# Kernel tuning notes

Measured on AMD Instinct MI355X. Metric: run time of the kernel, lower is better.

Reference implementation:

```python
import jax, jax.numpy as jnp
import numpy as np

D, N, L = 1024, 128, 128
B, S = 4, 4096

def setup_inputs() -> dict:
    key = jax.random.key(0)
    kx, kq, kk, kv = jax.random.split(key, 4)
    x = jax.random.normal(kx, (B, S, D), dtype=jnp.float32)
    # nn.Linear(d, n, bias=False) weight has shape [n, d]; y = x @ W.T
    Wq = jax.random.normal(kq, (N, D), dtype=jnp.float32) * (1.0 / np.sqrt(D))
    Wk = jax.random.normal(kk, (N, D), dtype=jnp.float32) * (1.0 / np.sqrt(D))
    Wv = jax.random.normal(kv, (L, D), dtype=jnp.float32) * (1.0 / np.sqrt(D))
    return {"x": x, "Wq": Wq, "Wk": Wk, "Wv": Wv}

def reference(x, Wq, Wk, Wv):
    scale = jnp.sqrt(jnp.asarray(D, dtype=x.dtype))  # self.d = sqrt(d) in source
    q = jnp.einsum('bsd,nd->bsn', x, Wq)  # [B,S,N]
    k = jnp.einsum('bsd,nd->bsn', x, Wk)  # [B,S,N]
    v = jnp.einsum('bsd,ld->bsl', x, Wv)  # [B,S,L]
    scores = jnp.einsum('bqn,bkn->bqk', q, k) / scale  # [B,S,S]
    a = jax.nn.softmax(scores, axis=-1)
    return jnp.einsum('bqk,bkl->bql', a, v)  # [B,S,L]
```

## Files before the change

### kernel.cpp

```cpp
#include <hip/hip_runtime.h>
#include <stdint.h>

typedef __attribute__((ext_vector_type(8))) _Float16 f16x8;
typedef __attribute__((ext_vector_type(4))) float f32x4;
typedef __attribute__((ext_vector_type(2))) float f32x2;

#define S_ 4096
#define D_ 1024
#define NROWS 16384
#define QSCALE 0.045084220f
#define EXP2(x) __builtin_amdgcn_exp2f(x)

__global__ __launch_bounds__(256) void cvtw(
    const float* __restrict__ Wq, const float* __restrict__ Wk,
    const float* __restrict__ Wv, _Float16* __restrict__ Wh)
{
  int i = (blockIdx.x * 256 + threadIdx.x) * 8;
  const float* src = (i < 131072) ? Wq : ((i < 262144) ? Wk : Wv);
  int off = i & 131071;
  f32x4 a = *(const f32x4*)(src + off);
  f32x4 b = *(const f32x4*)(src + off + 4);
  f16x8 h;
  #pragma unroll
  for (int j = 0; j < 4; ++j) { h[j] = (_Float16)a[j]; h[j + 4] = (_Float16)b[j]; }
  *(f16x8*)(Wh + i) = h;
}

__global__ __launch_bounds__(256) void gemm_qkv(
    const float* __restrict__ x, const _Float16* __restrict__ Wh,
    _Float16* __restrict__ qk, _Float16* __restrict__ vt)
{
  __shared__ char smem[32768];
  char* Ab[2] = { smem,        smem + 16384 };
  char* Bb[2] = { smem + 8192, smem + 24576 };
  const int tid  = threadIdx.x;
  const int lane = tid & 63, wid = tid >> 6;
  const int g = lane >> 4, l15 = lane & 15;
  const int m0 = blockIdx.x * 64;
  const int by = blockIdx.y;

  const char* pA[2];
  #pragma unroll
  for (int it = 0; it < 2; ++it) {
    int G = it * 256 + tid, row = G >> 3, gg = (G & 7) ^ (row & 7);
    pA[it] = (const char*)x + (size_t)(m0 + row) * 4096 + gg * 16;
  }
  const char* pB[2];
  #pragma unroll
  for (int it = 0; it < 2; ++it) {
    int d = it * 256 + tid;
    int rowhi = d >> 4, tt = (d & 15) ^ (rowhi & 15);
    int row = rowhi * 4 + (tt >> 2), gg = tt & 3;
    pB[it] = (const char*)(Wh + (size_t)by * 131072 + (size_t)row * 1024) + gg * 16;
  }

#define GSTAGE(bi) do {                                                        \
    _Pragma("unroll")                                                          \
    for (int it_ = 0; it_ < 2; ++it_) {                                        \
      __builtin_amdgcn_global_load_lds(pA[it_],                                \
          Ab[bi] + it_ * 4096 + wid * 1024, 16, 0, 0);                         \
      pA[it_] += 128;                                                          \
      __builtin_amdgcn_global_load_lds(pB[it_],                                \
          Bb[bi] + it_ * 4096 + wid * 1024, 16, 0, 0);                         \
      pB[it_] += 64;                                                           \
    }                                                                          \
  } while (0)

  f32x4 acc[4][2] = {};

#define GCOMPUTE(bi) do {                                                      \
    f16x8 af[4], bg[2];                                                        \
    _Pragma("unroll")                                                          \
    for (int mt = 0; mt < 4; ++mt) {                                           \
      int row = mt * 16 + l15;                                                 \
      const char* base = Ab[bi] + row * 128;                                   \
      f32x4 a0 = *(const f32x4*)(base + (((2 * g    ) ^ (row & 7)) << 4));     \
      f32x4 a1 = *(const f32x4*)(base + (((2 * g + 1) ^ (row & 7)) << 4));     \
      _Pragma("unroll")                                                        \
      for (int i = 0; i < 4; ++i) {                                            \
        af[mt][i] = (_Float16)a0[i]; af[mt][i + 4] = (_Float16)a1[i];          \
      }                                                                        \
    }                                                                          \
    _Pragma("unroll")                                                          \
    for (int nt = 0; nt < 2; ++nt) {                                           \
      int row = wid * 32 + nt * 16 + l15;                                      \
      int byte = ((row >> 2) * 256) +                                          \
                 (((((row & 3) << 2) | g) ^ ((row >> 2) & 15)) << 4);          \
      bg[nt] = *(const f16x8*)(Bb[bi] + byte);                                 \
    }                                                                          \
    __builtin_amdgcn_s_setprio(1);                                             \
    _Pragma("unroll")                                                          \
    for (int mt = 0; mt < 4; ++mt)                                             \
      _Pragma("unroll")                                                        \
      for (int nt = 0; nt < 2; ++nt)                                           \
        acc[mt][nt] = __builtin_amdgcn_mfma_f32_16x16x32_f16(af[mt], bg[nt],   \
                                                             acc[mt][nt], 0, 0, 0); \
    __builtin_amdgcn_s_setprio(0);                                             \
  } while (0)

  GSTAGE(0);
  __syncthreads();
  for (int t = 0; t < 32; t += 2) {
    GSTAGE(1);
    GCOMPUTE(0);
    __syncthreads();
    if (t + 2 < 32) GSTAGE(0);
    GCOMPUTE(1);
    __syncthreads();
  }

  if (by < 2) {
    const float sc = (by == 0) ? QSCALE : 1.0f;
    #pragma unroll
    for (int mt = 0; mt < 4; ++mt)
      #pragma unroll
      for (int nt = 0; nt < 2; ++nt)
        #pragma unroll
        for (int r = 0; r < 4; ++r) {
          int row = m0 + mt * 16 + (g << 2) + r;
          int col = by * 128 + wid * 32 + nt * 16 + l15;
          qk[(size_t)row * 256 + col] = (_Float16)(acc[mt][nt][r] * sc);
        }
  } else {
    _Float16* T = (_Float16*)smem;
    #pragma unroll
    for (int mt = 0; mt < 4; ++mt)
      #pragma unroll
      for (int nt = 0; nt < 2; ++nt)
        #pragma unroll
        for (int r = 0; r < 4; ++r)
          T[(mt * 16 + (g << 2) + r) * 128 + wid * 32 + nt * 16 + l15] =
              (_Float16)acc[mt][nt][r];
    __syncthreads();
    const int b = m0 >> 12, s_base = m0 & 4095;
    #pragma unroll
    for (int it = 0; it < 4; ++it) {
      int Wn = it * 256 + tid;
      int f = Wn >> 3, gran = Wn & 7;
      int kk = gran >> 2, q = gran & 3;
      f16x8 v;
      #pragma unroll
      for (int i = 0; i < 8; ++i) {
        int h = i >> 2, j = i & 3;
        v[i] = T[(kk * 32 + h * 16 + q * 4 + j) * 128 + f];
      }
      *(f16x8*)((char*)vt + (size_t)(b * 128 + f) * 8192 + s_base * 2 + gran * 16) = v;
    }
  }
#undef GSTAGE
#undef GCOMPUTE
}

__global__ __launch_bounds__(256, 2) void attn(const _Float16* __restrict__ qk,
                                               const _Float16* __restrict__ vt,
                                               _Float16* __restrict__ pO,
                                               float* __restrict__ pml,
                                               int ntiles)
{
  __shared__ _Float16 K0l[64 * 128], K1l[64 * 128];
  __shared__ _Float16 V0l[64 * 128], V1l[64 * 128];
  const int tid  = threadIdx.x;
  const int lane = tid & 63, wid = tid >> 6;
  const int g = lane >> 4, l15 = lane & 15;
  const int b  = blockIdx.y;
  const int q0 = blockIdx.x * 128;
  const int split = blockIdx.z;
  const int kv_begin = split * (ntiles * 64);

  f16x8 qf0[4], qf1[4];
  {
    const size_t qr0 = (size_t)(b * S_ + q0 + wid * 32 + l15) * 256;
    #pragma unroll
    for (int kk = 0; kk < 4; ++kk) {
      qf0[kk] = *(const f16x8*)(qk + qr0 + kk * 32 + g * 8);
      qf1[kk] = *(const f16x8*)(qk + qr0 + 16 * 256 + kk * 32 + g * 8);
    }
  }

  const char* gK[4]; const char* gV[4];
  #pragma unroll
  for (int it = 0; it < 4; ++it) {
    int G = it * 256 + tid;
    int row = G >> 4, ch = G & 15;
    gK[it] = (const char*)qk + (size_t)(b * S_ + kv_begin + row) * 512 + 256 +
             (((ch << 4)) ^ ((row & 15) << 4));
    int f = G >> 3, c = G & 7;
    gV[it] = (const char*)vt + (size_t)(b * 128 + f) * 8192 + (kv_begin >> 6) * 128 +
             ((c ^ (f & 7)) << 4);
  }

#define STAGE(Kb, Vb) do {                                                          \
    _Pragma("unroll")                                                               \
    for (int it_ = 0; it_ < 4; ++it_) {                                             \
      __builtin_amdgcn_global_load_lds(gK[it_],                                     \
          (char*)(Kb) + (it_ * 256 + wid * 64) * 16, 16, 0, 0);                     \
      __builtin_amdgcn_global_load_lds(gV[it_],                                     \
          (char*)(Vb) + (it_ * 256 + wid * 64) * 16, 16, 0, 0);                     \
      gK[it_] += 32768; gV[it_] += 128;                                             \
    }                                                                               \
  } while (0)

  f32x4 oa0[8] = {}, oa1[8] = {};
  float m0r = -1e30f, l0r = 0.f, m1r = -1e30f, l1r = 0.f;

#define COMPUTE(Kb, Vb) do {                                                        \
    f32x4 s0[4] = {}, s1[4] = {};                                                   \
    __builtin_amdgcn_s_setprio(1);                                                  \
    _Pragma("unroll")                                                               \
    for (int kk = 0; kk < 4; ++kk) {                                                \
      const char* kb = (const char*)(Kb) + l15 * 256 +                              \
                       (((kk << 6) | (g << 4)) ^ (l15 << 4));                       \
      _Pragma("unroll")                                                             \
      for (int kvt = 0; kvt < 4; ++kvt) {                                           \
        f16x8 kf = *(const f16x8*)(kb + kvt * 4096);                                \
        s0[kvt] = __builtin_amdgcn_mfma_f32_16x16x32_f16(kf, qf0[kk], s0[kvt],      \
                                                         0, 0, 0);                  \
        s1[kvt] = __builtin_amdgcn_mfma_f32_16x16x32_f16(kf, qf1[kk], s1[kvt],      \
                                                         0, 0, 0);                  \
      }                                                                             \
    }                                                                               \
    __builtin_amdgcn_s_setprio(0);                                                  \
    float p0 = fmaxf(                                                               \
        fmaxf(fmaxf(fmaxf(s0[0][0], s0[0][1]), fmaxf(s0[0][2], s0[0][3])),          \
              fmaxf(fmaxf(s0[1][0], s0[1][1]), fmaxf(s0[1][2], s0[1][3]))),         \
        fmaxf(fmaxf(fmaxf(s0[2][0], s0[2][1]), fmaxf(s0[2][2], s0[2][3])),          \
              fmaxf(fmaxf(s0[3][0], s0[3][1]), fmaxf(s0[3][2], s0[3][3]))));        \
    float p1 = fmaxf(                                                               \
        fmaxf(fmaxf(fmaxf(s1[0][0], s1[0][1]), fmaxf(s1[0][2], s1[0][3])),          \
              fmaxf(fmaxf(s1[1][0], s1[1][1]), fmaxf(s1[1][2], s1[1][3]))),         \
        fmaxf(fmaxf(fmaxf(s1[2][0], s1[2][1]), fmaxf(s1[2][2], s1[2][3])),          \
              fmaxf(fmaxf(s1[3][0], s1[3][1]), fmaxf(s1[3][2], s1[3][3]))));        \
    p0 = fmaxf(p0, __shfl_xor(p0, 16)); p0 = fmaxf(p0, __shfl_xor(p0, 32));         \
    p1 = fmaxf(p1, __shfl_xor(p1, 16)); p1 = fmaxf(p1, __shfl_xor(p1, 32));         \
    if (!__all((p0 - m0r <= 8.0f) && (p1 - m1r <= 8.0f))) {                         \
      float mn0 = fmaxf(m0r, p0), mn1 = fmaxf(m1r, p1);                             \
      float c0 = EXP2(m0r - mn0), c1 = EXP2(m1r - mn1);                             \
      l0r *= c0; m0r = mn0; l1r *= c1; m1r = mn1;                                   \
      _Pragma("unroll")                                                             \
      for (int r = 0; r < 4; ++r) {                                                 \
        int ad = ((g << 2) + r) << 2;                                               \
        float cr0 = __builtin_bit_cast(float,                                       \
            __builtin_amdgcn_ds_bpermute(ad, __builtin_bit_cast(int, c0)));         \
        float cr1 = __builtin_bit_cast(float,                                       \
            __builtin_amdgcn_ds_bpermute(ad, __builtin_bit_cast(int, c1)));         \
        _Pragma("unroll")                                                           \
        for (int ft = 0; ft < 8; ++ft) {                                            \
          oa0[ft][r] *= cr0; oa1[ft][r] *= cr1;                                     \
        }                                                                           \
      }                                                                             \
    }                                                                               \
    float ps0 = 0.f, ps1 = 0.f;                                                     \
    f16x8 pa0[2], pa1[2];                                                           \
    _Pragma("unroll")                                                               \
    for (int k2 = 0; k2 < 2; ++k2)                                                  \
      _Pragma("unroll")                                                             \
      for (int i = 0; i < 8; ++i) {                                                 \
        float e0 = EXP2(s0[2 * k2 + (i >> 2)][i & 3] - m0r);                        \
        float e1 = EXP2(s1[2 * k2 + (i >> 2)][i & 3] - m1r);                        \
        ps0 += e0; ps1 += e1;                                                       \
        pa0[k2][i] = (_Float16)e0; pa1[k2][i] = (_Float16)e1;                       \
      }                                                                             \
    ps0 += __shfl_xor(ps0, 16); ps0 += __shfl_xor(ps0, 32);                         \
    ps1 += __shfl_xor(ps1, 16); ps1 += __shfl_xor(ps1, 32);                         \
    l0r += ps0; l1r += ps1;                                                         \
    __builtin_amdgcn_s_setprio(1);                                                  \
    _Pragma("unroll")                                                               \
    for (int k2 = 0; k2 < 2; ++k2) {                                                \
      const char* vb = (const char*)(Vb) + l15 * 128 +                              \
                       (((k2 << 6) | (g << 4)) ^ ((l15 & 7) << 4));                 \
      _Pragma("unroll")                                                             \
      for (int ft = 0; ft < 8; ++ft) {                                              \
        f16x8 vf = *(const f16x8*)(vb + ft * 2048);                                 \
        oa0[ft] = __builtin_amdgcn_mfma_f32_16x16x32_f16(pa0[k2], vf, oa0[ft],      \
                                                         0, 0, 0);                  \
        oa1[ft] = __builtin_amdgcn_mfma_f32_16x16x32_f16(pa1[k2], vf, oa1[ft],      \
                                                         0, 0, 0);                  \
      }                                                                             \
    }                                                                               \
    __builtin_amdgcn_s_setprio(0);                                                  \
  } while (0)

  STAGE(K0l, V0l);
  __syncthreads();
  for (int t = 0; t < ntiles; t += 2) {
    STAGE(K1l, V1l);
    COMPUTE(K0l, V0l);
    __syncthreads();
    if (t + 2 < ntiles) STAGE(K0l, V0l);
    COMPUTE(K1l, V1l);
    __syncthreads();
  }

  #pragma unroll
  for (int s = 0; s < 2; ++s) {
    float mrun = s ? m1r : m0r, lrun = s ? l1r : l0r;
    f32x4* oa = s ? oa1 : oa0;
    #pragma unroll
    for (int r = 0; r < 4; ++r) {
      int ad = ((g << 2) + r) << 2;
      float mr = __builtin_bit_cast(float,
                   __builtin_amdgcn_ds_bpermute(ad, __builtin_bit_cast(int, mrun)));
      float lr = __builtin_bit_cast(float,
                   __builtin_amdgcn_ds_bpermute(ad, __builtin_bit_cast(int, lrun)));
      float inv = 1.f / lr;
      const int grow = b * S_ + q0 + wid * 32 + s * 16 + (g << 2) + r;
      _Float16* od = pO + ((size_t)split * NROWS + grow) * 128;
      #pragma unroll
      for (int ft = 0; ft < 8; ++ft)
        od[ft * 16 + l15] = (_Float16)(oa[ft][r] * inv);
      if (l15 == 0)
        *(f32x2*)(pml + ((size_t)split * NROWS + grow) * 2) = f32x2{mr, lr};
    }
  }
#undef STAGE
#undef COMPUTE
}

__global__ __launch_bounds__(256) void combine(const _Float16* __restrict__ pO,
                                               const float* __restrict__ pml,
                                               float* __restrict__ out,
                                               int nsplit)
{
  const int tid  = threadIdx.x;
  const int row  = blockIdx.x * 16 + (tid >> 4);
  const int colg = (tid & 15) * 8;

  float M = -1e30f;
  for (int s = 0; s < nsplit; ++s)
    M = fmaxf(M, pml[((size_t)s * NROWS + row) * 2]);
  float den = 0.f;
  float num[8] = {};
  for (int s = 0; s < nsplit; ++s) {
    f32x2 ml = *(const f32x2*)(pml + ((size_t)s * NROWS + row) * 2);
    float w = EXP2(ml.x - M) * ml.y;
    den += w;
    f16x8 o = *(const f16x8*)(pO + ((size_t)s * NROWS + row) * 128 + colg);
    #pragma unroll
    for (int j = 0; j < 8; ++j) num[j] += w * (float)o[j];
  }
  float inv = 1.f / den;
  f32x4 o0, o1;
  #pragma unroll
  for (int j = 0; j < 4; ++j) { o0[j] = num[j] * inv; o1[j] = num[4 + j] * inv; }
  *(f32x4*)(out + (size_t)row * 128 + colg)     = o0;
  *(f32x4*)(out + (size_t)row * 128 + colg + 4) = o1;
}

extern "C" void kernel_launch(void* const* d_in, const int* in_sizes, int n_in,
                              void* d_out, int out_size, void* d_ws, size_t ws_size,
                              hipStream_t stream)
{
  (void)in_sizes; (void)n_in; (void)out_size;
  const float* x  = (const float*)d_in[0];
  const float* Wq = (const float*)d_in[1];
  const float* Wk = (const float*)d_in[2];
  const float* Wv = (const float*)d_in[3];

  char* ws = (char*)d_ws;
  _Float16* qkbuf = (_Float16*)ws;
  _Float16* vtbuf = (_Float16*)(ws + (size_t)NROWS * 256 * 2);
  const size_t base  = (size_t)NROWS * 256 * 2 + (size_t)4 * 128 * 4096 * 2;
  const size_t perO  = (size_t)NROWS * 128 * 2;
  const size_t perML = (size_t)NROWS * 2 * 4;

  int nsplit = 4;
  while (nsplit > 1 && base + (size_t)nsplit * (perO + perML) > ws_size) nsplit >>= 1;

  _Float16* Whb = (_Float16*)(ws + base);
  _Float16* pO  = (_Float16*)(ws + base);
  float*    pml = (float*)(ws + base + (size_t)nsplit * perO);
  float*    out = (float*)d_out;

  cvtw<<<192, 256, 0, stream>>>(Wq, Wk, Wv, Whb);
  dim3 gg(256, 3);
  gemm_qkv<<<gg, 256, 0, stream>>>(x, Whb, qkbuf, vtbuf);
  dim3 ga(S_ / 128, 4, nsplit);
  attn<<<ga, 256, 0, stream>>>(qkbuf, vtbuf, pO, pml, 64 / nsplit);
  combine<<<NROWS / 16, 256, 0, stream>>>(pO, pml, out, nsplit);
}
```

Baseline: 83.04 us.

## Compute softmax row sums via MFMA with ones and split tile into halves

The softmax denominator is now accumulated by an extra MFMA that multiplies the fp16 probabilities by a vector of ones. This replaces the per-lane float sums and their cross-lane shuffle reductions. Each 64-key tile is also processed as two 32-key halves, each with its own max, rescale and PV step, which lowers live score registers but doubles the max-reduction and rescale checks. The sum now comes from fp16-rounded probabilities, which can shift accuracy slightly, and each half adds two MFMAs.

After: 84.65 us. Within noise of the previous version (+1.9%).

```diff
diff --git a/kernel.cpp b/kernel.cpp
--- a/kernel.cpp
+++ b/kernel.cpp
@@ -176,6 +176,9 @@
       qf1[kk] = *(const f16x8*)(qk + qr0 + 16 * 256 + kk * 32 + g * 8);
     }
   }
+  f16x8 ones;
+  #pragma unroll
+  for (int i = 0; i < 8; ++i) ones[i] = (_Float16)1.0f;
 
   const char* gK[4]; const char* gV[4];
   #pragma unroll
@@ -201,83 +204,73 @@
   } while (0)
 
   f32x4 oa0[8] = {}, oa1[8] = {};
-  float m0r = -1e30f, l0r = 0.f, m1r = -1e30f, l1r = 0.f;
+  f32x4 oL0 = {}, oL1 = {};
+  float m0r = -1e30f, m1r = -1e30f;
 
 #define COMPUTE(Kb, Vb) do {                                                        \
-    f32x4 s0[4] = {}, s1[4] = {};                                                   \
-    __builtin_amdgcn_s_setprio(1);                                                  \
     _Pragma("unroll")                                                               \
-    for (int kk = 0; kk < 4; ++kk) {                                                \
-      const char* kb = (const char*)(Kb) + l15 * 256 +                              \
-                       (((kk << 6) | (g << 4)) ^ (l15 << 4));                       \
+    for (int k2 = 0; k2 < 2; ++k2) {                                                \
+      f32x4 s0[2] = {}, s1[2] = {};                                                 \
+      __builtin_amdgcn_s_setprio(1);                                                \
       _Pragma("unroll")                                                             \
-      for (int kvt = 0; kvt < 4; ++kvt) {                                           \
-        f16x8 kf = *(const f16x8*)(kb + kvt * 4096);                                \
-        s0[kvt] = __builtin_amdgcn_mfma_f32_16x16x32_f16(kf, qf0[kk], s0[kvt],      \
-                                                         0, 0, 0);                  \
-        s1[kvt] = __builtin_amdgcn_mfma_f32_16x16x32_f16(kf, qf1[kk], s1[kvt],      \
-                                                         0, 0, 0);                  \
-      }                                                                             \
-    }                                                                               \
-    __builtin_amdgcn_s_setprio(0);                                                  \
-    float p0 = fmaxf(                                                               \
-        fmaxf(fmaxf(fmaxf(s0[0][0], s0[0][1]), fmaxf(s0[0][2], s0[0][3])),          \
-              fmaxf(fmaxf(s0[1][0], s0[1][1]), fmaxf(s0[1][2], s0[1][3]))),         \
-        fmaxf(fmaxf(fmaxf(s0[2][0], s0[2][1]), fmaxf(s0[2][2], s0[2][3])),          \
-              fmaxf(fmaxf(s0[3][0], s0[3][1]), fmaxf(s0[3][2], s0[3][3]))));        \
-    float p1 = fmaxf(                                                               \
-        fmaxf(fmaxf(fmaxf(s1[0][0], s1[0][1]), fmaxf(s1[0][2], s1[0][3])),          \
-              fmaxf(fmaxf(s1[1][0], s1[1][1]), fmaxf(s1[1][2], s1[1][3]))),         \
-        fmaxf(fmaxf(fmaxf(s1[2][0], s1[2][1]), fmaxf(s1[2][2], s1[2][3])),          \
-              fmaxf(fmaxf(s1[3][0], s1[3][1]), fmaxf(s1[3][2], s1[3][3]))));        \
-    p0 = fmaxf(p0, __shfl_xor(p0, 16)); p0 = fmaxf(p0, __shfl_xor(p0, 32));         \
-    p1 = fmaxf(p1, __shfl_xor(p1, 16)); p1 = fmaxf(p1, __shfl_xor(p1, 32));         \
-    if (!__all((p0 - m0r <= 8.0f) && (p1 - m1r <= 8.0f))) {                         \
-      float mn0 = fmaxf(m0r, p0), mn1 = fmaxf(m1r, p1);                             \
-      float c0 = EXP2(m0r - mn0), c1 = EXP2(m1r - mn1);                             \
-      l0r *= c0; m0r = mn0; l1r *= c1; m1r = mn1;                                   \
-      _Pragma("unroll")                                                             \
-      for (int r = 0; r < 4; ++r) {                                                 \
-        int ad = ((g << 2) + r) << 2;                                               \
-        float cr0 = __builtin_bit_cast(float,                                       \
-            __builtin_amdgcn_ds_bpermute(ad, __builtin_bit_cast(int, c0)));         \
-        float cr1 = __builtin_bit_cast(float,                                       \
-            __builtin_amdgcn_ds_bpermute(ad, __builtin_bit_cast(int, c1)));         \
+      for (int kk = 0; kk < 4; ++kk) {                                              \
+        const char* kb = (const char*)(Kb) + l15 * 256 +                            \
+                         (((kk << 6) | (g << 4)) ^ (l15 << 4));                     \
         _Pragma("unroll")                                                           \
-        for (int ft = 0; ft < 8; ++ft) {                                            \
-          oa0[ft][r] *= cr0; oa1[ft][r] *= cr1;                                     \
+        for (int k1 = 0; k1 < 2; ++k1) {                                            \
+          f16x8 kf = *(const f16x8*)(kb + (2 * k2 + k1) * 4096);                    \
+          s0[k1] = __builtin_amdgcn_mfma_f32_16x16x32_f16(kf, qf0[kk], s0[k1],      \
+                                                          0, 0, 0);                 \
+          s1[k1] = __builtin_amdgcn_mfma_f32_16x16x32_f16(kf, qf1[kk], s1[k1],      \
+                                                          0, 0, 0);                 \
         }                                                                           \
       }                                                                             \
-    }                                                                               \
-    float ps0 = 0.f, ps1 = 0.f;                                                     \
-    f16x8 pa0[2], pa1[2];                                                           \
-    _Pragma("unroll")                                                               \
-    for (int k2 = 0; k2 < 2; ++k2)                                                  \
+      __builtin_amdgcn_s_setprio(0);                                                \
+      float p0 = fmaxf(fmaxf(fmaxf(s0[0][0], s0[0][1]), fmaxf(s0[0][2], s0[0][3])), \
+                       fmaxf(fmaxf(s0[1][0], s0[1][1]), fmaxf(s0[1][2], s0[1][3])));\
+      float p1 = fmaxf(fmaxf(fmaxf(s1[0][0], s1[0][1]), fmaxf(s1[0][2], s1[0][3])), \
+                       fmaxf(fmaxf(s1[1][0], s1[1][1]), fmaxf(s1[1][2], s1[1][3])));\
+      p0 = fmaxf(p0, __shfl_xor(p0, 16)); p0 = fmaxf(p0, __shfl_xor(p0, 32));       \
+      p1 = fmaxf(p1, __shfl_xor(p1, 16)); p1 = fmaxf(p1, __shfl_xor(p1, 32));       \
+      if (!__all((p0 - m0r <= 8.0f) && (p1 - m1r <= 8.0f))) {                       \
+        float mn0 = fmaxf(m0r, p0), mn1 = fmaxf(m1r, p1);                           \
+        float c0 = EXP2(m0r - mn0), c1 = EXP2(m1r - mn1);                           \
+        m0r = mn0; m1r = mn1;                                                       \
+        _Pragma("unroll")                                                           \
+        for (int r = 0; r < 4; ++r) {                                               \
+          int ad = ((g << 2) + r) << 2;                                             \
+          float cr0 = __builtin_bit_cast(float,                                     \
+              __builtin_amdgcn_ds_bpermute(ad, __builtin_bit_cast(int, c0)));       \
+          float cr1 = __builtin_bit_cast(float,                                     \
+              __builtin_amdgcn_ds_bpermute(ad, __builtin_bit_cast(int, c1)));       \
+          _Pragma("unroll")                                                         \
+          for (int ft = 0; ft < 8; ++ft) {                                          \
+            oa0[ft][r] *= cr0; oa1[ft][r] *= cr1;                                   \
+          }                                                                         \
+          oL0[r] *= cr0; oL1[r] *= cr1;                                             \
+        }                                                                           \
+      }                                                                             \
+      f16x8 pa0, pa1;                                                               \
       _Pragma("unroll")                                                             \
       for (int i = 0; i < 8; ++i) {                                                 \
-        float e0 = EXP2(s0[2 * k2 + (i >> 2)][i & 3] - m0r);                        \
-        float e1 = EXP2(s1[2 * k2 + (i >> 2)][i & 3] - m1r);                        \
-        ps0 += e0; ps1 += e1;                                                       \
-        pa0[k2][i] = (_Float16)e0; pa1[k2][i] = (_Float16)e1;                       \
+        pa0[i] = (_Float16)EXP2(s0[i >> 2][i & 3] - m0r);                           \
+        pa1[i] = (_Float16)EXP2(s1[i >> 2][i & 3] - m1r);                           \
       }                                                                             \
-    ps0 += __shfl_xor(ps0, 16); ps0 += __shfl_xor(ps0, 32);                         \
-    ps1 += __shfl_xor(ps1, 16); ps1 += __shfl_xor(ps1, 32);                         \
-    l0r += ps0; l1r += ps1;                                                         \
-    __builtin_amdgcn_s_setprio(1);                                                  \
-    _Pragma("unroll")                                                               \
-    for (int k2 = 0; k2 < 2; ++k2) {                                                \
+      __builtin_amdgcn_s_setprio(1);                                                \
       const char* vb = (const char*)(Vb) + l15 * 128 +                              \
                        (((k2 << 6) | (g << 4)) ^ ((l15 & 7) << 4));                 \
       _Pragma("unroll")                                                             \
       for (int ft = 0; ft < 8; ++ft) {                                              \
         f16x8 vf = *(const f16x8*)(vb + ft * 2048);                                 \
-        oa0[ft] = __builtin_amdgcn_mfma_f32_16x16x32_f16(pa0[k2], vf, oa0[ft],      \
+        oa0[ft] = __builtin_amdgcn_mfma_f32_16x16x32_f16(pa0, vf, oa0[ft],          \
                                                          0, 0, 0);                  \
-        oa1[ft] = __builtin_amdgcn_mfma_f32_16x16x32_f16(pa1[k2], vf, oa1[ft],      \
+        oa1[ft] = __builtin_amdgcn_mfma_f32_16x16x32_f16(pa1, vf, oa1[ft],          \
                                                          0, 0, 0);                  \
       }                                                                             \
+      oL0 = __builtin_amdgcn_mfma_f32_16x16x32_f16(pa0, ones, oL0, 0, 0, 0);        \
+      oL1 = __builtin_amdgcn_mfma_f32_16x16x32_f16(pa1, ones, oL1, 0, 0, 0);        \
+      __builtin_amdgcn_s_setprio(0);                                                \
     }                                                                               \
-    __builtin_amdgcn_s_setprio(0);                                                  \
   } while (0)
 
   STAGE(K0l, V0l);
@@ -293,15 +286,15 @@
 
   #pragma unroll
   for (int s = 0; s < 2; ++s) {
-    float mrun = s ? m1r : m0r, lrun = s ? l1r : l0r;
+    float mrun = s ? m1r : m0r;
     f32x4* oa = s ? oa1 : oa0;
+    f32x4 oL  = s ? oL1 : oL0;
     #pragma unroll
     for (int r = 0; r < 4; ++r) {
       int ad = ((g << 2) + r) << 2;
       float mr = __builtin_bit_cast(float,
                    __builtin_amdgcn_ds_bpermute(ad, __builtin_bit_cast(int, mrun)));
-      float lr = __builtin_bit_cast(float,
-                   __builtin_amdgcn_ds_bpermute(ad, __builtin_bit_cast(int, lrun)));
+      float lr = oL[r];
       float inv = 1.f / lr;
       const int grow = b * S_ + q0 + wid * 32 + s * 16 + (g << 2) + r;
       _Float16* od = pO + ((size_t)split * NROWS + grow) * 128;
```
